# Kernel tuning notes

Hardware: AMD Instinct MI355X
Metric: run time of the kernel (lower is better)

Reference implementation:

```python
import jax, jax.numpy as jnp
import numpy as np

COMMITMENT_COST = 0.25


def setup_inputs() -> dict:
    key = jax.random.key(0)
    k1, k2 = jax.random.split(key)
    B, H, W, D, K = 64, 32, 32, 64, 512
    inputs = jax.random.normal(k1, (B, H, W, D), dtype=jnp.float32)
    # VarianceScaling(): truncated normal with stddev ~ sqrt(1/fan_in); plain normal scaled is fine as init
    embeddings = jax.random.normal(k2, (D, K), dtype=jnp.float32) * np.float32(1.0 / np.sqrt(D))
    return {"inputs": inputs, "embeddings": embeddings}


def reference(inputs, embeddings):
    D = embeddings.shape[0]
    flat = inputs.reshape(-1, D)  # [N, D]
    distances = (
        jnp.sum(flat * flat, axis=1, keepdims=True)
        - 2.0 * (flat @ embeddings)
        + jnp.sum(embeddings * embeddings, axis=0, keepdims=True)
    )
    encoding_indices = jnp.argmin(distances, axis=1)  # [N]
    # one-hot @ embeddings.T is just a gather of rows of embeddings.T
    quantized = jnp.take(embeddings.T, encoding_indices, axis=0).reshape(inputs.shape)
    loss = (
        jnp.mean(jnp.square(jax.lax.stop_gradient(quantized) - inputs))
        + COMMITMENT_COST * jnp.mean(jnp.square(quantized - jax.lax.stop_gradient(inputs)))
    )
    # straight-through estimator
    quantized_st = inputs + jax.lax.stop_gradient(quantized - inputs)
    indices = encoding_indices.reshape(inputs.shape[:-1])
    return quantized_st, indices, loss
```

## Files before the change

kernel.cpp:

```cpp
#include <hip/hip_runtime.h>
#include <stdint.h>


#define DDIM 64
#define KCODES 512

typedef _Float16 f16x8 __attribute__((ext_vector_type(8)));
typedef float f32x4 __attribute__((ext_vector_type(4)));


__device__ __forceinline__ void split2(float f, _Float16& h1, _Float16& h2) {
  h1 = (_Float16)f;
  float r = f - (float)h1;
  h2 = (_Float16)r;
}

__global__ void vq_prep_m(const float* __restrict__ w,
                          f16x8* __restrict__ wb,
                          float* __restrict__ wT, float* __restrict__ wsq,
                          float* __restrict__ loss_out) {
  const int b = blockIdx.x, t = threadIdx.x;
  if (b < 16) {
    const int c = b * 256 + t;
    const int ctg = c >> 7;
    const int h = (c >> 6) & 1;
    const int L = c & 63, quad = L >> 4, col = L & 15;
    f16x8 v1, v2;
#pragma unroll
    for (int j = 0; j < 8; ++j) {
      float f = w[(quad * 8 + 32 * h + j) * KCODES + ctg * 16 + col];
      _Float16 h1, h2; split2(f, h1, h2);
      v1[j] = h1; v2[j] = h2;
    }
    const int base = ctg * 4 + h * 2;
    wb[(base + 0) * 64 + L] = v1;
    wb[(base + 1) * 64 + L] = v2;
  } else if (b < 144) {
    int g = (b - 16) * 256 + t;
    int d = g >> 9, k = g & 511;
    wT[k * DDIM + d] = w[g];
    if (g == 0) *loss_out = 0.f;
  } else {
    int i = (b - 144) * 256 + t;
    int k = i >> 2, p = i & 3;
    float s = 0.f;
#pragma unroll
    for (int dd = 0; dd < 16; ++dd) {
      float tv = w[(p * 16 + dd) * KCODES + k];
      s = fmaf(tv, tv, s);
    }
    s += __shfl_xor(s, 1, 64);
    s += __shfl_xor(s, 2, 64);
    if (p == 0) wsq[k] = s;
  }
}

__global__ __launch_bounds__(256, 2)
void vq_mfma(const float* __restrict__ x_in, const f16x8* __restrict__ wb,
             const float* __restrict__ wsq, const float* __restrict__ wT,
             float* __restrict__ out_q, float* __restrict__ out_idx,
             float* __restrict__ loss_out) {
  __shared__ unsigned long long sm_key[128];
  __shared__ float sm_xsq[128];
  __shared__ unsigned int sm_idx[128];
  __shared__ float sm_loss[128];

  const int t = threadIdx.x, b = blockIdx.x;
  const int wv = t >> 6, L = t & 63, quad = L >> 4, col = L & 15;

  f16x8 bb[2][4];
#pragma unroll
  for (int j = 0; j < 4; ++j) bb[0][j] = wb[j * 64 + L];

  f16x8 a[2][2][2];
#pragma unroll
  for (int as = 0; as < 2; ++as) {
    const float* xr =
        x_in + ((size_t)b * 128 + (wv * 2 + as) * 16 + col) * DDIM + quad * 8;
    float ssq = 0.f;
#pragma unroll
    for (int h = 0; h < 2; ++h) {
      float4 p0 = *(const float4*)(xr + 32 * h);
      float4 p1 = *(const float4*)(xr + 32 * h + 4);
      float f[8] = {p0.x, p0.y, p0.z, p0.w, p1.x, p1.y, p1.z, p1.w};
      f16x8 v1, v2;
#pragma unroll
      for (int j = 0; j < 8; ++j) {
        ssq = fmaf(f[j], f[j], ssq);
        _Float16 h1, h2; split2(f[j], h1, h2);
        v1[j] = h1; v2[j] = h2;
      }
      a[as][0][h] = v1; a[as][1][h] = v2;
    }
    ssq += __shfl_xor(ssq, 16, 64);
    ssq += __shfl_xor(ssq, 32, 64);
    if (quad == 0) sm_xsq[wv * 32 + as * 16 + col] = ssq;
  }

  float best[2][4];
  int bidx[2][4];
#pragma unroll
  for (int as = 0; as < 2; ++as)
#pragma unroll
    for (int r = 0; r < 4; ++r) { best[as][r] = 3.0e38f; bidx[as][r] = 0; }

#pragma unroll 2
  for (int kk = 0; kk < 32; ++kk) {
    const int cur = kk & 1, nxt = cur ^ 1;
    if (kk < 31) {
#pragma unroll
      for (int j = 0; j < 4; ++j)
        bb[nxt][j] = wb[(kk + 1) * 256 + j * 64 + L];
    }
    float wq = wsq[kk * 16 + col];

    f32x4 aA0 = {0.f, 0.f, 0.f, 0.f}, aB0 = {0.f, 0.f, 0.f, 0.f};
    f32x4 aA1 = {0.f, 0.f, 0.f, 0.f}, aB1 = {0.f, 0.f, 0.f, 0.f};
    {
      f16x8 b0 = bb[cur][0], b1 = bb[cur][1];
      aA0 = __builtin_amdgcn_mfma_f32_16x16x32_f16(a[0][0][0], b0, aA0, 0, 0, 0);
      aA1 = __builtin_amdgcn_mfma_f32_16x16x32_f16(a[1][0][0], b0, aA1, 0, 0, 0);
      aA0 = __builtin_amdgcn_mfma_f32_16x16x32_f16(a[0][0][0], b1, aA0, 0, 0, 0);
      aA1 = __builtin_amdgcn_mfma_f32_16x16x32_f16(a[1][0][0], b1, aA1, 0, 0, 0);
      aA0 = __builtin_amdgcn_mfma_f32_16x16x32_f16(a[0][1][0], b0, aA0, 0, 0, 0);
      aA1 = __builtin_amdgcn_mfma_f32_16x16x32_f16(a[1][1][0], b0, aA1, 0, 0, 0);
    }
    {
      f16x8 b2 = bb[cur][2], b3 = bb[cur][3];
      aB0 = __builtin_amdgcn_mfma_f32_16x16x32_f16(a[0][0][1], b2, aB0, 0, 0, 0);
      aB1 = __builtin_amdgcn_mfma_f32_16x16x32_f16(a[1][0][1], b2, aB1, 0, 0, 0);
      aB0 = __builtin_amdgcn_mfma_f32_16x16x32_f16(a[0][0][1], b3, aB0, 0, 0, 0);
      aB1 = __builtin_amdgcn_mfma_f32_16x16x32_f16(a[1][0][1], b3, aB1, 0, 0, 0);
      aB0 = __builtin_amdgcn_mfma_f32_16x16x32_f16(a[0][1][1], b2, aB0, 0, 0, 0);
      aB1 = __builtin_amdgcn_mfma_f32_16x16x32_f16(a[1][1][1], b2, aB1, 0, 0, 0);
    }
    f32x4 acc0 = aA0 + aB0;
    f32x4 acc1 = aA1 + aB1;
    int code = kk * 16 + col;
#pragma unroll
    for (int r = 0; r < 4; ++r) {
      float d0 = fmaf(acc0[r], -2.0f, wq);
      if (d0 < best[0][r]) { best[0][r] = d0; bidx[0][r] = code; }
      float d1 = fmaf(acc1[r], -2.0f, wq);
      if (d1 < best[1][r]) { best[1][r] = d1; bidx[1][r] = code; }
    }
  }

#pragma unroll
  for (int as = 0; as < 2; ++as) {
#pragma unroll
    for (int r = 0; r < 4; ++r) {
      unsigned int ub = __float_as_uint(best[as][r]);
      ub = (ub & 0x80000000u) ? ~ub : (ub | 0x80000000u);
      unsigned long long key = ((unsigned long long)ub << 32) |
                               (unsigned long long)(unsigned int)bidx[as][r];
#pragma unroll
      for (int off = 1; off < 16; off <<= 1) {
        unsigned long long o = __shfl_xor(key, off, 64);
        key = o < key ? o : key;
      }
      if (col == 0)
        sm_key[wv * 32 + as * 16 + quad * 4 + r] = key;
    }
  }
  __syncthreads();

  if (t < 128) {
    unsigned long long k = sm_key[t];
    unsigned int idx = (unsigned int)k;
    sm_idx[t] = idx;
    out_idx[(size_t)b * 128 + t] = (float)idx;
    unsigned int u = (unsigned int)(k >> 32);
    u = (u & 0x80000000u) ? (u & 0x7FFFFFFFu) : ~u;
    sm_loss[t] = (__uint_as_float(u) + sm_xsq[t]) * (1.25f / 4194304.0f);
  }
  __syncthreads();

  float4* dst = (float4*)(out_q + (size_t)b * 8192);
#pragma unroll
  for (int i = 0; i < 8; ++i) {
    int e4 = i * 256 + t;
    int p2 = e4 >> 4, d4 = e4 & 15;
    unsigned int idx = sm_idx[p2];
    dst[e4] = ((const float4*)(wT + (size_t)idx * DDIM))[d4];
  }

  if (t < 64) {
    float s = sm_loss[t] + sm_loss[t + 64];
#pragma unroll
    for (int off = 32; off > 0; off >>= 1) s += __shfl_down(s, off);
    if (t == 0) atomicAdd(loss_out, s);
  }
}


__global__ void vq_prep(const float* __restrict__ w, float* __restrict__ wT,
                        float* __restrict__ wsq, float* __restrict__ loss_out) {
  int g = blockIdx.x * 256 + threadIdx.x;
  int d = g >> 9, k = g & 511;
  wT[k * DDIM + d] = w[g];
  if (g < KCODES) {
    float s = 0.f;
    for (int dd = 0; dd < DDIM; ++dd) {
      float t = w[dd * KCODES + g];
      s = fmaf(t, t, s);
    }
    wsq[g] = s;
  }
  if (g == 0) *loss_out = 0.f;
}

__global__ __launch_bounds__(512, 8)
void vq_main(const float* __restrict__ x_in, const float* __restrict__ w,
             const float* __restrict__ wT, const float* __restrict__ wsq,
             float* __restrict__ out_q, float* __restrict__ out_idx,
             float* __restrict__ loss_out) {
  __shared__ float xs[DDIM][65];
  __shared__ unsigned long long sm_key[8][64];
  __shared__ unsigned int sm_idx[64];
  __shared__ float sm_sx[64];
  __shared__ float sm_loss[64];

  const int t = threadIdx.x;
  const int pb = blockIdx.x;
  const int wv = __builtin_amdgcn_readfirstlane(t >> 6);
  const int lane = t & 63;

  {
    const float4* src = (const float4*)(x_in + (size_t)pb * 4096);
#pragma unroll
    for (int i = 0; i < 2; ++i) {
      int e4 = i * 512 + t;
      float4 v = src[e4];
      int e = e4 << 2;
      int pt = e >> 6, d = e & 63;
      xs[d][pt] = v.x; xs[d + 1][pt] = v.y;
      xs[d + 2][pt] = v.z; xs[d + 3][pt] = v.w;
    }
  }
  __syncthreads();

  const int kbase = wv << 6;
  float best = 3.0e38f;
  int bidx = 0;
  float sx = 0.f;

#pragma unroll 1
  for (int kb = 0; kb < 2; ++kb) {
    const int k0 = kbase + (kb << 5);
    const float* wp = w + k0;
    float acc[32];
#pragma unroll
    for (int c = 0; c < 32; ++c) acc[c] = 0.f;
#pragma unroll 1
    for (int d8 = 0; d8 < 8; ++d8) {
      float xv[8];
#pragma unroll
      for (int dd = 0; dd < 8; ++dd) xv[dd] = xs[(d8 << 3) + dd][lane];
      if (wv == 0 && kb == 0) {
#pragma unroll
        for (int dd = 0; dd < 8; ++dd) sx = fmaf(xv[dd], xv[dd], sx);
      }
#pragma unroll
      for (int dd = 0; dd < 8; ++dd) {
        const float* wd = wp + (((d8 << 3) + dd) << 9);
#pragma unroll
        for (int c = 0; c < 32; ++c) acc[c] = fmaf(wd[c], xv[dd], acc[c]);
      }
    }
#pragma unroll
    for (int c = 0; c < 32; ++c) {
      float dist = fmaf(acc[c], -2.0f, wsq[k0 + c]);
      if (dist < best) { best = dist; bidx = k0 + c; }
    }
  }

  unsigned int ub = __float_as_uint(best);
  ub = (ub & 0x80000000u) ? ~ub : (ub | 0x80000000u);
  sm_key[wv][lane] =
      ((unsigned long long)ub << 32) | (unsigned long long)(unsigned int)bidx;
  if (wv == 0) sm_sx[lane] = sx;
  __syncthreads();

  if (t < 64) {
    unsigned long long k = sm_key[0][t];
#pragma unroll
    for (int wi = 1; wi < 8; ++wi) {
      unsigned long long k2 = sm_key[wi][t];
      k = k2 < k ? k2 : k;
    }
    unsigned int idx = (unsigned int)k;
    sm_idx[t] = idx;
    out_idx[((size_t)pb << 6) + t] = (float)idx;
    unsigned int u = (unsigned int)(k >> 32);
    u = (u & 0x80000000u) ? (u & 0x7FFFFFFFu) : ~u;
    sm_loss[t] = (__uint_as_float(u) + sm_sx[t]) * (1.25f / 4194304.0f);
  }
  __syncthreads();

  float4* dst = (float4*)(out_q + (size_t)pb * 4096);
#pragma unroll
  for (int i = 0; i < 2; ++i) {
    int e4 = i * 512 + t;
    int p2 = e4 >> 4, d4 = e4 & 15;
    unsigned int idx = sm_idx[p2];
    dst[e4] = ((const float4*)(wT + (size_t)idx * DDIM))[d4];
  }

  if (t < 64) {
    float s = sm_loss[t];
#pragma unroll
    for (int off = 32; off > 0; off >>= 1) s += __shfl_down(s, off);
    if (t == 0) atomicAdd(loss_out, s);
  }
}

extern "C" void kernel_launch(void* const* d_in, const int* in_sizes, int n_in,
                              void* d_out, int out_size, void* d_ws, size_t ws_size,
                              hipStream_t stream) {
  const float* x = (const float*)d_in[0];
  const float* w = (const float*)d_in[1];

  float* out_q = (float*)d_out;
  float* out_idx = out_q + 4194304;
  float* loss_out = out_q + 4259840;

  char* ws = (char*)d_ws;
  if (ws_size >= 264192) {
    f16x8* wbp = (f16x8*)(ws);
    float* wT = (float*)(ws + 131072);
    float* wsq = (float*)(ws + 262144);
    vq_prep_m<<<152, 256, 0, stream>>>(w, wbp, wT, wsq, loss_out);
    vq_mfma<<<512, 256, 0, stream>>>(x, wbp, wsq, wT, out_q, out_idx,
                                     loss_out);
  } else {
    float* wT = (float*)(ws);
    float* wsq = (float*)(ws + 131072);
    vq_prep<<<128, 256, 0, stream>>>(w, wT, wsq, loss_out);
    vq_main<<<1024, 512, 0, stream>>>(x, w, wT, wsq, out_q, out_idx,
                                      loss_out);
  }
}
```

Before: 93.07 us.

## Fuse codebook prep and VQ search into one cooperative kernel with grid sync

Merges the codebook preprocessing kernel and the MFMA nearest-code search into a single cooperative launch. Blocks first do the prep work and split their input rows into fp16 pairs, then a grid-wide sync makes the prepared codebook visible before the search. This removes one kernel launch and overlaps the input loads with the prep phase, at the cost of a grid barrier and a launch-bounds occupancy constraint. If the cooperative launch fails, the code falls back to the two-kernel path.

```diff
diff --git a/kernel.cpp b/kernel.cpp
--- a/kernel.cpp
+++ b/kernel.cpp
@@ -1,5 +1,8 @@
 #include <hip/hip_runtime.h>
+#include <hip/hip_cooperative_groups.h>
 #include <stdint.h>
+
+namespace cg = cooperative_groups;
 
 
 #define DDIM 64
@@ -14,6 +17,185 @@
   float r = f - (float)h1;
   h2 = (_Float16)r;
 }
+
+
+__global__ __launch_bounds__(256, 2)
+void vq_fused(const float* __restrict__ x_in, const float* __restrict__ w,
+              f16x8* __restrict__ wb, float* __restrict__ wT,
+              float* __restrict__ wsq, float* __restrict__ out_q,
+              float* __restrict__ out_idx, float* __restrict__ loss_out) {
+  __shared__ unsigned long long sm_key[128];
+  __shared__ float sm_xsq[128];
+  __shared__ unsigned int sm_idx[128];
+  __shared__ float sm_loss[128];
+
+  const int t = threadIdx.x, b = blockIdx.x;
+  const int wv = t >> 6, L = t & 63, quad = L >> 4, col = L & 15;
+
+  const int gid = b * 256 + t;
+  if (gid < 4096) {
+    const int c = gid;
+    const int ctg = c >> 7;
+    const int h = (c >> 6) & 1;
+    const int Lp = c & 63, qp = Lp >> 4, cp = Lp & 15;
+    f16x8 v1, v2;
+#pragma unroll
+    for (int j = 0; j < 8; ++j) {
+      float f = w[(qp * 8 + 32 * h + j) * KCODES + ctg * 16 + cp];
+      _Float16 h1, h2; split2(f, h1, h2);
+      v1[j] = h1; v2[j] = h2;
+    }
+    const int base = ctg * 4 + h * 2;
+    wb[(base + 0) * 64 + Lp] = v1;
+    wb[(base + 1) * 64 + Lp] = v2;
+  } else if (gid < 36864) {
+    int g = gid - 4096;
+    int d = g >> 9, k = g & 511;
+    wT[k * DDIM + d] = w[g];
+  } else if (gid < 38912) {
+    int i = gid - 36864;
+    int k = i >> 2, p = i & 3;
+    float s = 0.f;
+#pragma unroll
+    for (int dd = 0; dd < 16; ++dd) {
+      float tv = w[(p * 16 + dd) * KCODES + k];
+      s = fmaf(tv, tv, s);
+    }
+    s += __shfl_xor(s, 1, 64);
+    s += __shfl_xor(s, 2, 64);
+    if (p == 0) wsq[k] = s;
+  } else if (gid == 38912) {
+    *loss_out = 0.f;
+  }
+
+  f16x8 a[2][2][2];
+#pragma unroll
+  for (int as = 0; as < 2; ++as) {
+    const float* xr =
+        x_in + ((size_t)b * 128 + (wv * 2 + as) * 16 + col) * DDIM + quad * 8;
+    float ssq = 0.f;
+#pragma unroll
+    for (int h = 0; h < 2; ++h) {
+      float4 p0 = *(const float4*)(xr + 32 * h);
+      float4 p1 = *(const float4*)(xr + 32 * h + 4);
+      float f[8] = {p0.x, p0.y, p0.z, p0.w, p1.x, p1.y, p1.z, p1.w};
+      f16x8 v1, v2;
+#pragma unroll
+      for (int j = 0; j < 8; ++j) {
+        ssq = fmaf(f[j], f[j], ssq);
+        _Float16 h1, h2; split2(f[j], h1, h2);
+        v1[j] = h1; v2[j] = h2;
+      }
+      a[as][0][h] = v1; a[as][1][h] = v2;
+    }
+    ssq += __shfl_xor(ssq, 16, 64);
+    ssq += __shfl_xor(ssq, 32, 64);
+    if (quad == 0) sm_xsq[wv * 32 + as * 16 + col] = ssq;
+  }
+
+  __threadfence();
+  cg::this_grid().sync();
+
+  f16x8 bb[2][4];
+#pragma unroll
+  for (int j = 0; j < 4; ++j) bb[0][j] = wb[j * 64 + L];
+
+  float best[2][4];
+  int bidx[2][4];
+#pragma unroll
+  for (int as = 0; as < 2; ++as)
+#pragma unroll
+    for (int r = 0; r < 4; ++r) { best[as][r] = 3.0e38f; bidx[as][r] = 0; }
+
+#pragma unroll 2
+  for (int kk = 0; kk < 32; ++kk) {
+    const int cur = kk & 1, nxt = cur ^ 1;
+    if (kk < 31) {
+#pragma unroll
+      for (int j = 0; j < 4; ++j)
+        bb[nxt][j] = wb[(kk + 1) * 256 + j * 64 + L];
+    }
+    float wq = wsq[kk * 16 + col];
+
+    f32x4 aA0 = {0.f, 0.f, 0.f, 0.f}, aB0 = {0.f, 0.f, 0.f, 0.f};
+    f32x4 aA1 = {0.f, 0.f, 0.f, 0.f}, aB1 = {0.f, 0.f, 0.f, 0.f};
+    {
+      f16x8 b0 = bb[cur][0], b1 = bb[cur][1];
+      aA0 = __builtin_amdgcn_mfma_f32_16x16x32_f16(a[0][0][0], b0, aA0, 0, 0, 0);
+      aA1 = __builtin_amdgcn_mfma_f32_16x16x32_f16(a[1][0][0], b0, aA1, 0, 0, 0);
+      aA0 = __builtin_amdgcn_mfma_f32_16x16x32_f16(a[0][0][0], b1, aA0, 0, 0, 0);
+      aA1 = __builtin_amdgcn_mfma_f32_16x16x32_f16(a[1][0][0], b1, aA1, 0, 0, 0);
+      aA0 = __builtin_amdgcn_mfma_f32_16x16x32_f16(a[0][1][0], b0, aA0, 0, 0, 0);
+      aA1 = __builtin_amdgcn_mfma_f32_16x16x32_f16(a[1][1][0], b0, aA1, 0, 0, 0);
+    }
+    {
+      f16x8 b2 = bb[cur][2], b3 = bb[cur][3];
+      aB0 = __builtin_amdgcn_mfma_f32_16x16x32_f16(a[0][0][1], b2, aB0, 0, 0, 0);
+      aB1 = __builtin_amdgcn_mfma_f32_16x16x32_f16(a[1][0][1], b2, aB1, 0, 0, 0);
+      aB0 = __builtin_amdgcn_mfma_f32_16x16x32_f16(a[0][0][1], b3, aB0, 0, 0, 0);
+      aB1 = __builtin_amdgcn_mfma_f32_16x16x32_f16(a[1][0][1], b3, aB1, 0, 0, 0);
+      aB0 = __builtin_amdgcn_mfma_f32_16x16x32_f16(a[0][1][1], b2, aB0, 0, 0, 0);
+      aB1 = __builtin_amdgcn_mfma_f32_16x16x32_f16(a[1][1][1], b2, aB1, 0, 0, 0);
+    }
+    f32x4 acc0 = aA0 + aB0;
+    f32x4 acc1 = aA1 + aB1;
+    int code = kk * 16 + col;
+#pragma unroll
+    for (int r = 0; r < 4; ++r) {
+      float d0 = fmaf(acc0[r], -2.0f, wq);
+      if (d0 < best[0][r]) { best[0][r] = d0; bidx[0][r] = code; }
+      float d1 = fmaf(acc1[r], -2.0f, wq);
+      if (d1 < best[1][r]) { best[1][r] = d1; bidx[1][r] = code; }
+    }
+  }
+
+#pragma unroll
+  for (int as = 0; as < 2; ++as) {
+#pragma unroll
+    for (int r = 0; r < 4; ++r) {
+      unsigned int ub = __float_as_uint(best[as][r]);
+      ub = (ub & 0x80000000u) ? ~ub : (ub | 0x80000000u);
+      unsigned long long key = ((unsigned long long)ub << 32) |
+                               (unsigned long long)(unsigned int)bidx[as][r];
+#pragma unroll
+      for (int off = 1; off < 16; off <<= 1) {
+        unsigned long long o = __shfl_xor(key, off, 64);
+        key = o < key ? o : key;
+      }
+      if (col == 0)
+        sm_key[wv * 32 + as * 16 + quad * 4 + r] = key;
+    }
+  }
+  __syncthreads();
+
+  if (t < 128) {
+    unsigned long long k = sm_key[t];
+    unsigned int idx = (unsigned int)k;
+    sm_idx[t] = idx;
+    out_idx[(size_t)b * 128 + t] = (float)idx;
+    unsigned int u = (unsigned int)(k >> 32);
+    u = (u & 0x80000000u) ? (u & 0x7FFFFFFFu) : ~u;
+    sm_loss[t] = (__uint_as_float(u) + sm_xsq[t]) * (1.25f / 4194304.0f);
+  }
+  __syncthreads();
+
+  float4* dst = (float4*)(out_q + (size_t)b * 8192);
+#pragma unroll
+  for (int i = 0; i < 8; ++i) {
+    int e4 = i * 256 + t;
+    int p2 = e4 >> 4, d4 = e4 & 15;
+    unsigned int idx = sm_idx[p2];
+    dst[e4] = ((const float4*)(wT + (size_t)idx * DDIM))[d4];
+  }
+
+  if (t < 64) {
+    float s = sm_loss[t] + sm_loss[t + 64];
+#pragma unroll
+    for (int off = 32; off > 0; off >>= 1) s += __shfl_down(s, off);
+    if (t == 0) atomicAdd(loss_out, s);
+  }
+}
+
 
 __global__ void vq_prep_m(const float* __restrict__ w,
                           f16x8* __restrict__ wb,
@@ -330,9 +512,16 @@
     f16x8* wbp = (f16x8*)(ws);
     float* wT = (float*)(ws + 131072);
     float* wsq = (float*)(ws + 262144);
-    vq_prep_m<<<152, 256, 0, stream>>>(w, wbp, wT, wsq, loss_out);
-    vq_mfma<<<512, 256, 0, stream>>>(x, wbp, wsq, wT, out_q, out_idx,
-                                     loss_out);
+    void* args[] = {(void*)&x,     (void*)&w,       (void*)&wbp,
+                    (void*)&wT,    (void*)&wsq,     (void*)&out_q,
+                    (void*)&out_idx, (void*)&loss_out};
+    hipError_t err = hipLaunchCooperativeKernel(
+        (void*)vq_fused, dim3(512), dim3(256), args, 0, stream);
+    if (err != hipSuccess) {
+      vq_prep_m<<<152, 256, 0, stream>>>(w, wbp, wT, wsq, loss_out);
+      vq_mfma<<<512, 256, 0, stream>>>(x, wbp, wsq, wT, out_q, out_idx,
+                                       loss_out);
+    }
   } else {
     float* wT = (float*)(ws);
     float* wsq = (float*)(ws + 131072);
```

Result: slower. 164.8 us (+77.1%).
